# Performance work log

Hardware: AMD Instinct MI355X
Metric: run time of the kernel (lower is better)

## Reference

```python
import jax, jax.numpy as jnp
import numpy as np

INPUT_SIZE = 32   # activity vocab
HIDDEN = 512
OUT = 33          # OUT-1 activity logits + 1 duration
COND = 128
LAYERS = 2
MAXLEN = 64
BATCH = 256
SOS = 0
SLOPE = 0.01      # LeakyReLU default negative slope

def _leaky(x):
    return jnp.where(x >= 0, x, SLOPE * x)

def setup_inputs() -> dict:
    key = jax.random.key(0)
    ks = jax.random.split(key, 16)
    s = 0.05  # small init scale keeps gates in a sane range
    return {
        "batch_size": BATCH,
        "h0": jax.random.normal(ks[0], (LAYERS, BATCH, HIDDEN), jnp.float32),
        "c0": jax.random.normal(ks[1], (LAYERS, BATCH, HIDDEN), jnp.float32),
        "conditionals": jax.random.normal(ks[2], (BATCH, COND), jnp.float32),
        "emb": jax.random.normal(ks[3], (INPUT_SIZE, HIDDEN - 1), jnp.float32) * s,
        "Wih": jax.random.normal(ks[4], (LAYERS, 4 * HIDDEN, HIDDEN), jnp.float32) * s,
        "Whh": jax.random.normal(ks[5], (LAYERS, 4 * HIDDEN, HIDDEN), jnp.float32) * s,
        "bih": jax.random.normal(ks[6], (LAYERS, 4 * HIDDEN), jnp.float32) * s,
        "bhh": jax.random.normal(ks[7], (LAYERS, 4 * HIDDEN), jnp.float32) * s,
        "fcW": jax.random.normal(ks[8], (HIDDEN, COND), jnp.float32) * s,
        "fcb": jax.random.normal(ks[9], (HIDDEN,), jnp.float32) * s,
        "fc2W": jax.random.normal(ks[10], (HIDDEN, HIDDEN), jnp.float32) * s,
        "fc2b": jax.random.normal(ks[11], (HIDDEN,), jnp.float32) * s,
        "fc3W": jax.random.normal(ks[12], (OUT, HIDDEN), jnp.float32) * s,
        "fc3b": jax.random.normal(ks[13], (OUT,), jnp.float32) * s,
    }

def reference(batch_size, h0, c0, conditionals, emb, Wih, Whh, bih, bhh,
              fcW, fcb, fc2W, fc2b, fc3W, fc3b):
    B = h0.shape[1]
    # conditionals branch is step-invariant: compute once (same math as per-step fc+LeakyReLU)
    cond = _leaky(conditionals @ fcW.T + fcb)  # [B, H]
    # decoder_input = zeros[B,1,2] with act channel = sos
    inp0 = jnp.concatenate(
        [jnp.full((B, 1), float(SOS), jnp.float32), jnp.zeros((B, 1), jnp.float32)], axis=-1)

    def step(carry, _):
        h, c, inp = carry  # h,c: [L,B,H], inp: [B,2]
        # CustomDurationEmbedding: embed act index, concat duration channel -> [B,H]
        x = jnp.concatenate([emb[inp[:, 0].astype(jnp.int32)], inp[:, 1:]], axis=-1)
        hs, cs = [], []
        for l in range(LAYERS):  # seq_len==1 per step -> one LSTM cell per layer
            g = x @ Wih[l].T + bih[l] + h[l] @ Whh[l].T + bhh[l]  # [B,4H]
            i_g, f_g, g_g, o_g = jnp.split(g, 4, axis=-1)         # torch gate order i,f,g,o
            c_l = jax.nn.sigmoid(f_g) * c[l] + jax.nn.sigmoid(i_g) * jnp.tanh(g_g)
            h_l = jax.nn.sigmoid(o_g) * jnp.tanh(c_l)
            hs.append(h_l); cs.append(c_l)
            x = h_l
        h_new, c_new = jnp.stack(hs), jnp.stack(cs)
        # conditional_add: (lstm_out + cond) -> fc2 -> LeakyReLU -> fc3
        pred = _leaky((x + cond) @ fc2W.T + fc2b) @ fc3W.T + fc3b  # [B,OUT]
        # pack: topk(1) over activity logits; softmax over singleton seq dim == 1.0
        act = jnp.argmax(pred[:, :OUT - 1], axis=-1).astype(pred.dtype)[:, None]
        dur = jnp.ones((B, 1), pred.dtype)
        nxt = jnp.concatenate([act, dur], axis=-1)
        return (h_new, c_new, nxt), pred

    _, outs = jax.lax.scan(step, (h0, c0, inp0), None, length=MAXLEN)  # [T,B,OUT]
    outs = jnp.transpose(outs, (1, 0, 2))  # [B,T,OUT]
    acts_log_probs = jax.nn.log_softmax(outs[..., :OUT - 1], axis=-1)
    durations = jax.nn.softmax(outs[..., OUT - 1:], axis=1)  # Softmax(dim=-2): over time
    return jnp.concatenate([acts_log_probs, durations], axis=-1)
```

## Files before the change

### kernel.cpp

```cpp
#include <hip/hip_runtime.h>
#include <math.h>

#define BB   256
#define HH   512
#define TT   64
#define NOUT 33
#define CD   128
#define NTHR 1024
#define NWG  256
#define LOFF (4*HH*HH)
#define SZ   (HH*BB)
#define FC2OFF 4194304

typedef float f16v __attribute__((ext_vector_type(16)));
typedef const __attribute__((address_space(4))) float cfloat;
typedef const __attribute__((address_space(4))) f16v  cf16v;

__device__ __forceinline__ float sigm(float x)  { return 1.0f/(1.0f+expf(-x)); }
__device__ __forceinline__ float lrelu(float x) { return x >= 0.0f ? x : 0.01f*x; }

__device__ __forceinline__ float gld(const float* p) {
  return __hip_atomic_load(p, __ATOMIC_RELAXED, __HIP_MEMORY_SCOPE_AGENT);
}
__device__ __forceinline__ float2 gld2(const float* p) {
  unsigned long long v = __hip_atomic_load((const unsigned long long*)p,
                                           __ATOMIC_RELAXED, __HIP_MEMORY_SCOPE_AGENT);
  union { unsigned long long u; float2 f; } c; c.u = v; return c.f;
}
__device__ __forceinline__ void gst(float* p, float v) {
  __hip_atomic_store(p, v, __ATOMIC_RELAXED, __HIP_MEMORY_SCOPE_AGENT);
}
__device__ __forceinline__ unsigned gldu(const unsigned* p) {
  return __hip_atomic_load(p, __ATOMIC_RELAXED, __HIP_MEMORY_SCOPE_AGENT);
}

__device__ __forceinline__ cfloat* cptr(const float* p) {
  unsigned long long u = (unsigned long long)p;
  unsigned lo = __builtin_amdgcn_readfirstlane((unsigned)u);
  unsigned hi = __builtin_amdgcn_readfirstlane((unsigned)(u >> 32));
  return (cfloat*)((((unsigned long long)hi) << 32) | (unsigned long long)lo);
}

__device__ __forceinline__ void gbar(unsigned* bar, unsigned ep, int grp, bool fence) {
  __syncthreads();
  if (threadIdx.x == 0) {
    if (fence) __builtin_amdgcn_fence(__ATOMIC_RELEASE, "agent");
    unsigned old = __hip_atomic_fetch_add(&bar[grp*16], 1u, __ATOMIC_RELAXED, __HIP_MEMORY_SCOPE_AGENT);
    if (old == ep*32u + 31u) {
      unsigned o2 = __hip_atomic_fetch_add(&bar[128], 1u, __ATOMIC_RELAXED, __HIP_MEMORY_SCOPE_AGENT);
      if (o2 == ep*8u + 7u)
        __hip_atomic_store(&bar[144], ep+1u, __ATOMIC_RELAXED, __HIP_MEMORY_SCOPE_AGENT);
    }
    while (gldu(&bar[144]) < ep+1u) __builtin_amdgcn_s_sleep(1);
    if (fence) __builtin_amdgcn_fence(__ATOMIC_ACQUIRE, "agent");
  }
  __syncthreads();
}

extern "C" __global__ void __launch_bounds__(256)
transpose_weights(const float* __restrict__ Wih, const float* __restrict__ Whh,
                  const float* __restrict__ fc2W, float* __restrict__ wsT)
{
  const int i = blockIdx.x, tid = threadIdx.x;
  float* dst = wsT + (size_t)i*32768;
  #pragma unroll 1
  for (int idx = tid; idx < 32768; idx += 256) {
    int slot = idx & 15, k = (idx>>4)&511, rh = (idx>>13)&1, l = (idx>>14)&1;
    int a = slot>>3, r = slot&7, u = r>>2, g = r&3;
    int hu = i*4 + rh*2 + u;
    const float* src = a ? Whh : Wih;
    dst[idx] = src[(size_t)l*LOFF + (size_t)(g*HH+hu)*HH + k];
  }
  float* dstf = wsT + FC2OFF + (size_t)i*2048;
  #pragma unroll 1
  for (int idx = tid; idx < 2048; idx += 256) {
    int r = idx & 3, k = idx >> 2;
    dstf[idx] = fc2W[(size_t)(i*4+r)*HH + k];
  }
}

__device__ __forceinline__ void lstm_phase(const float* __restrict__ wTl,
    const float* __restrict__ bias, float* __restrict__ red,
    const float* __restrict__ xsrc, const float* __restrict__ hsrc,
    float* __restrict__ hdst, float& creg, int i, int j, int tid)
{
  const int lane = tid & 63, wvid = tid >> 6;
  const int rh = wvid & 1, ks = wvid >> 1;
  cf16v* wp = (cf16v*)cptr(wTl + ((size_t)rh*512 + ks*64)*16);
  const int bo = j*128 + 2*lane;
  const float* xp = xsrc + (size_t)(ks*64)*BB + bo;
  const float* hp = hsrc + (size_t)(ks*64)*BB + bo;

  float acc[16];
  #pragma unroll
  for (int r = 0; r < 16; ++r) acc[r] = 0.f;

  float2 qx[2], qh[2], px[2], ph[2], rx[2], rhb[2];
  #pragma unroll
  for (int kk = 0; kk < 2; ++kk) { qx[kk]=gld2(xp+kk*BB);     qh[kk]=gld2(hp+kk*BB); }
  #pragma unroll
  for (int kk = 0; kk < 2; ++kk) { px[kk]=gld2(xp+(2+kk)*BB); ph[kk]=gld2(hp+(2+kk)*BB); }

  #pragma unroll 1
  for (int g = 0; g < 32; ++g) {
    if (g+2 < 32) {
      #pragma unroll
      for (int kk = 0; kk < 2; ++kk) {
        rx[kk]  = gld2(xp + (g*2+4+kk)*BB);
        rhb[kk] = gld2(hp + (g*2+4+kk)*BB);
      }
    }
    #pragma unroll
    for (int kk = 0; kk < 2; ++kk) {
      f16v w = wp[g*2+kk];
      float2 xv = qx[kk], hv = qh[kk];
      #pragma unroll
      for (int r = 0; r < 8; ++r) {
        acc[r*2+0] += w[r]*xv.x + w[8+r]*hv.x;
        acc[r*2+1] += w[r]*xv.y + w[8+r]*hv.y;
      }
    }
    #pragma unroll
    for (int kk = 0; kk < 2; ++kk) {
      qx[kk]=px[kk]; qh[kk]=ph[kk]; px[kk]=rx[kk]; ph[kk]=rhb[kk];
    }
  }
  #pragma unroll
  for (int r = 0; r < 8; ++r)
    *(float2*)(red + (size_t)(ks*16 + rh*8 + r)*128 + 2*lane) = make_float2(acc[r*2], acc[r*2+1]);
  __syncthreads();
  if (tid < 512) {
    const int lhu = tid >> 7, b = tid & 127;
    float g4[4];
    #pragma unroll
    for (int gg = 0; gg < 4; ++gg) {
      float s = bias[lhu*4+gg];
      #pragma unroll
      for (int q = 0; q < 8; ++q) s += red[(q*16 + lhu*4+gg)*128 + b];
      g4[gg] = s;
    }
    float ig=sigm(g4[0]), fg=sigm(g4[1]), gv=tanhf(g4[2]), og=sigm(g4[3]);
    float cn = fg*creg + ig*gv;
    creg = cn;
    gst(hdst + (size_t)(i*4+lhu)*BB + j*128 + b, og*tanhf(cn));
  }
}

__device__ __forceinline__ void fc2_phase(const float* __restrict__ h2src,
    const float* __restrict__ wsTf, float* __restrict__ yb,
    const float* lds_bc, const float* condY_l, float* __restrict__ red,
    int i, int j, int tid)
{
  const int lane = tid & 63, ks2 = tid >> 6;
  cf16v* wp = (cf16v*)cptr(wsTf + (size_t)ks2*128);
  const int bo = j*128 + 2*lane;
  const float* hp = h2src + (size_t)(ks2*32)*BB + bo;
  float acc[8];
  #pragma unroll
  for (int r = 0; r < 8; ++r) acc[r] = 0.f;
  float2 qh[4], ph[4];
  #pragma unroll
  for (int kk = 0; kk < 4; ++kk) qh[kk] = gld2(hp + kk*BB);
  #pragma unroll 1
  for (int g = 0; g < 8; ++g) {
    if (g+1 < 8) {
      #pragma unroll
      for (int kk = 0; kk < 4; ++kk) ph[kk] = gld2(hp + (g*4+4+kk)*BB);
    }
    f16v w = wp[g];
    #pragma unroll
    for (int kk = 0; kk < 4; ++kk) {
      float2 hv = qh[kk];
      #pragma unroll
      for (int r = 0; r < 4; ++r) {
        acc[r*2+0] += w[kk*4+r]*hv.x;
        acc[r*2+1] += w[kk*4+r]*hv.y;
      }
    }
    #pragma unroll
    for (int kk = 0; kk < 4; ++kk) qh[kk] = ph[kk];
  }
  #pragma unroll
  for (int r = 0; r < 4; ++r)
    *(float2*)(red + (size_t)(ks2*4+r)*128 + 2*lane) = make_float2(acc[r*2], acc[r*2+1]);
  __syncthreads();
  if (tid < 512) {
    int r = tid >> 7, b = tid & 127;
    float s = lds_bc[r] + condY_l[r*128+b];
    #pragma unroll
    for (int q = 0; q < 16; ++q) s += red[(q*4+r)*128 + b];
    gst(yb + (size_t)(i*4+r)*BB + j*128 + b, lrelu(s));
  }
}

extern "C" __global__ void __launch_bounds__(NTHR)
decoder_kernel(const float* __restrict__ h0, const float* __restrict__ c0,
               const float* __restrict__ conds, const float* __restrict__ emb,
               const float* __restrict__ wsTW, const float* __restrict__ bih,
               const float* __restrict__ bhh, const float* __restrict__ fcW,
               const float* __restrict__ fcb, const float* __restrict__ fc2W,
               const float* __restrict__ fc2b, const float* __restrict__ fc3W,
               const float* __restrict__ fc3b,
               float* __restrict__ out, unsigned* bar, float* wsf)
{
  const int w = blockIdx.x;
  const int i = w & 127, j = w >> 7;
  const int grp = w & 7;
  const int tid = threadIdx.x;

  float* xbuf  = wsf;
  float* h1a = wsf + 1*SZ;  float* h1b = wsf + 2*SZ;
  float* h2a = wsf + 3*SZ;  float* h2b = wsf + 4*SZ;
  float* yb  = wsf + 5*SZ;
  float* condb = wsf + 6*SZ;
  const float* wTi  = wsTW + (size_t)i*32768;
  const float* wsTf = wsTW + FC2OFF + (size_t)i*2048;

  __shared__ float red[16384];
  __shared__ float lds_y[HH];
  __shared__ float part[NOUT][17];
  __shared__ float condY_l[512];
  __shared__ float lds_b1[16], lds_b2[16], lds_bc[4];
  __shared__ int   lds_act;
  __shared__ float lds_pad[3072];
  if (tid == 0) ((volatile float*)lds_pad)[0] = 0.f;

  if (tid < 16) {
    int u2 = tid >> 2, g = tid & 3;
    int hu = i*4 + u2;
    lds_b1[tid] = bih[g*HH+hu] + bhh[g*HH+hu];
    lds_b2[tid] = bih[4*HH + g*HH+hu] + bhh[4*HH + g*HH+hu];
  }
  if (tid < 4) lds_bc[tid] = fc2b[i*4 + tid];

  {
    int u = tid >> 8, b = tid & 255;
    int hug = i*4 + u;
    h1a[(size_t)hug*BB + b] = h0[(size_t)b*HH + hug];
    h2a[(size_t)hug*BB + b] = h0[(size_t)(BB+b)*HH + hug];
    xbuf[(size_t)hug*BB + b] = (hug < HH-1) ? emb[hug] : 0.0f;
    const float* crow = conds + (size_t)b*CD;
    cfloat* fr = cptr(fcW + (size_t)hug*CD);
    float s = fcb[hug];
    #pragma unroll 4
    for (int q = 0; q < CD; q += 4)
      s += fr[q]*crow[q] + fr[q+1]*crow[q+1] + fr[q+2]*crow[q+2] + fr[q+3]*crow[q+3];
    condb[(size_t)hug*BB + b] = lrelu(s);
  }
  float c1 = 0.f, c2 = 0.f;
  if (tid < 512) {
    int lhu = tid >> 7, b = tid & 127;
    int hug = i*4 + lhu, bg = j*128 + b;
    c1 = c0[(size_t)bg*HH + hug];
    c2 = c0[(size_t)(BB+bg)*HH + hug];
  }
  unsigned ep = 0;
  gbar(bar, ep++, grp, true);

  if (tid < 512) {
    int r = tid >> 7, b = tid & 127, bg = j*128 + b;
    cfloat* wr = cptr(fc2W + (size_t)(i*4+r)*HH);
    float s = 0.f;
    #pragma unroll 4
    for (int k = 0; k < HH; ++k) s += wr[k]*condb[(size_t)k*BB + bg];
    condY_l[r*128 + b] = s;
  }
  __syncthreads();

  for (int t = 0; t < TT; ++t) {
    float* h1r = (t&1) ? h1b : h1a;  float* h1w = (t&1) ? h1a : h1b;
    float* h2r = (t&1) ? h2b : h2a;  float* h2w = (t&1) ? h2a : h2b;

    lstm_phase(wTi,         lds_b1, red, xbuf, h1r, h1w, c1, i, j, tid);
    gbar(bar, ep++, grp, false);
    lstm_phase(wTi + 16384, lds_b2, red, h1w, h2r, h2w, c2, i, j, tid);
    gbar(bar, ep++, grp, false);
    fc2_phase(h2w, wsTf, yb, lds_bc, condY_l, red, i, j, tid);
    gbar(bar, ep++, grp, false);
    {
      if (tid < 512) lds_y[tid] = gld(yb + (size_t)tid*BB + w);
      __syncthreads();
      int o = 0, kc = 0;
      bool active = false;
      if (tid < 512)      { o = tid & 31; kc = tid >> 5; active = true; }
      else if (tid < 528) { o = 32;       kc = tid - 512; active = true; }
      if (active) {
        float p = 0.f;
        const float* fw = fc3W + (size_t)o*HH + kc*32;
        #pragma unroll
        for (int k2 = 0; k2 < 32; ++k2) p += fw[k2] * lds_y[kc*32 + k2];
        part[o][kc] = p;
      }
      __syncthreads();
      float predv = -1e30f;
      if (tid < NOUT) {
        float s = fc3b[tid];
        #pragma unroll
        for (int kc2 = 0; kc2 < 16; ++kc2) s += part[tid][kc2];
        predv = s;
        out[(size_t)(w*TT + t)*NOUT + tid] = s;
      }
      if (tid < 64) {
        float v  = (tid < 32) ? predv : -1e30f;
        int  idx = tid;
        #pragma unroll
        for (int off = 32; off > 0; off >>= 1) {
          float ov = __shfl_xor(v, off);
          int   oi = __shfl_xor(idx, off);
          if (ov > v || (ov == v && oi < idx)) { v = ov; idx = oi; }
        }
        if (tid == 0) lds_act = idx;
      }
      __syncthreads();
      const int act = lds_act;
      if (tid < 512)
        gst(xbuf + (size_t)tid*BB + w, (tid < HH-1) ? emb[(size_t)act*(HH-1) + tid] : 1.0f);
    }
    gbar(bar, ep++, grp, false);
  }

  if (tid < TT) {
    const int s = tid;
    float* po = out + (size_t)(w*TT + s)*NOUT;
    float v[NOUT];
    #pragma unroll
    for (int o = 0; o < NOUT; ++o) v[o] = po[o];
    float m = v[0];
    #pragma unroll
    for (int o = 1; o < 32; ++o) m = fmaxf(m, v[o]);
    float sum = 0.f;
    #pragma unroll
    for (int o = 0; o < 32; ++o) sum += expf(v[o] - m);
    float lse = m + logf(sum);
    #pragma unroll
    for (int o = 0; o < 32; ++o) po[o] = v[o] - lse;
    float d = v[32];
    float dm = d;
    #pragma unroll
    for (int off = 32; off > 0; off >>= 1) dm = fmaxf(dm, __shfl_xor(dm, off));
    float e = expf(d - dm);
    float es = e;
    #pragma unroll
    for (int off = 32; off > 0; off >>= 1) es += __shfl_xor(es, off);
    po[32] = e / es;
  }
}

extern "C" void kernel_launch(void* const* d_in, const int* in_sizes, int n_in,
                              void* d_out, int out_size, void* d_ws, size_t ws_size,
                              hipStream_t stream) {
  const float* h0   = (const float*)d_in[1];
  const float* c0   = (const float*)d_in[2];
  const float* cnd  = (const float*)d_in[3];
  const float* emb  = (const float*)d_in[4];
  const float* Wih  = (const float*)d_in[5];
  const float* Whh  = (const float*)d_in[6];
  const float* bih  = (const float*)d_in[7];
  const float* bhh  = (const float*)d_in[8];
  const float* fcW  = (const float*)d_in[9];
  const float* fcb  = (const float*)d_in[10];
  const float* fc2W = (const float*)d_in[11];
  const float* fc2b = (const float*)d_in[12];
  const float* fc3W = (const float*)d_in[13];
  const float* fc3b = (const float*)d_in[14];

  unsigned* bar = (unsigned*)d_ws;
  float* wsf = (float*)((char*)d_ws + 1024);
  float* wsT = wsf + 7*SZ;

  (void)hipMemsetAsync(d_ws, 0, 1024, stream);

  hipLaunchKernelGGL(transpose_weights, dim3(128), dim3(256), 0, stream,
                     Wih, Whh, fc2W, wsT);
  hipLaunchKernelGGL(decoder_kernel, dim3(NWG), dim3(NTHR), 0, stream,
                     h0, c0, cnd, emb, wsT, bih, bhh, fcW, fcb,
                     fc2W, fc2b, fc3W, fc3b, (float*)d_out, bar, wsf);
}
```

Measured before the change: 4.567 ms.

## Give each wave all 16 gate rows over a 32-wide K slice in LSTM matvec

The LSTM phase stops splitting gate rows across two waves. Each of 16 waves now computes all 16 gate rows for a 32-element K slice, which halves the redundant x/h activation loads per wave. The weight transpose layout is changed to match, and the reduction now sums 16 partials instead of 8, so the LDS red buffer doubles to 128KB. The fc2 phase is reworked to stream 8-float weight vectors with a two-row h prefetch. The cost is 32 accumulators per thread, more register pressure, and a larger LDS footprint in place of the old padding array.

```diff
diff --git a/kernel.cpp b/kernel.cpp
--- a/kernel.cpp
+++ b/kernel.cpp
@@ -13,8 +13,10 @@
 #define FC2OFF 4194304
 
 typedef float f16v __attribute__((ext_vector_type(16)));
+typedef float f8v  __attribute__((ext_vector_type(8)));
 typedef const __attribute__((address_space(4))) float cfloat;
 typedef const __attribute__((address_space(4))) f16v  cf16v;
+typedef const __attribute__((address_space(4))) f8v   cf8v;
 
 __device__ __forceinline__ float sigm(float x)  { return 1.0f/(1.0f+expf(-x)); }
 __device__ __forceinline__ float lrelu(float x) { return x >= 0.0f ? x : 0.01f*x; }
@@ -65,9 +67,9 @@
   float* dst = wsT + (size_t)i*32768;
   #pragma unroll 1
   for (int idx = tid; idx < 32768; idx += 256) {
-    int slot = idx & 15, k = (idx>>4)&511, rh = (idx>>13)&1, l = (idx>>14)&1;
-    int a = slot>>3, r = slot&7, u = r>>2, g = r&3;
-    int hu = i*4 + rh*2 + u;
+    int slot = idx & 31, k = (idx>>5)&511, l = idx>>14;
+    int a = slot>>4, r = slot&15, u = r>>2, g = r&3;
+    int hu = i*4 + u;
     const float* src = a ? Whh : Wih;
     dst[idx] = src[(size_t)l*LOFF + (size_t)(g*HH+hu)*HH + k];
   }
@@ -84,50 +86,47 @@
     const float* __restrict__ xsrc, const float* __restrict__ hsrc,
     float* __restrict__ hdst, float& creg, int i, int j, int tid)
 {
-  const int lane = tid & 63, wvid = tid >> 6;
-  const int rh = wvid & 1, ks = wvid >> 1;
-  cf16v* wp = (cf16v*)cptr(wTl + ((size_t)rh*512 + ks*64)*16);
+  const int lane = tid & 63, ks = tid >> 6;
+  cf16v* wp = (cf16v*)cptr(wTl + (size_t)(ks*32)*32);
   const int bo = j*128 + 2*lane;
-  const float* xp = xsrc + (size_t)(ks*64)*BB + bo;
-  const float* hp = hsrc + (size_t)(ks*64)*BB + bo;
-
-  float acc[16];
+  const float* xp = xsrc + (size_t)(ks*32)*BB + bo;
+  const float* hp = hsrc + (size_t)(ks*32)*BB + bo;
+
+  float acc[32];
   #pragma unroll
-  for (int r = 0; r < 16; ++r) acc[r] = 0.f;
-
-  float2 qx[2], qh[2], px[2], ph[2], rx[2], rhb[2];
+  for (int r = 0; r < 32; ++r) acc[r] = 0.f;
+
+  float2 qx0, qh0, qx1, qh1, nx0, nh0, nx1, nh1;
+  qx0 = gld2(xp);      qh0 = gld2(hp);
+  qx1 = gld2(xp + BB); qh1 = gld2(hp + BB);
+
+  #pragma unroll 1
+  for (int it = 0; it < 16; ++it) {
+    if (it+1 < 16) {
+      nx0 = gld2(xp + (2*it+2)*BB); nh0 = gld2(hp + (2*it+2)*BB);
+      nx1 = gld2(xp + (2*it+3)*BB); nh1 = gld2(hp + (2*it+3)*BB);
+    }
+    {
+      f16v wi = wp[it*4+0], wh = wp[it*4+1];
+      #pragma unroll
+      for (int r = 0; r < 16; ++r) {
+        acc[2*r]   += wi[r]*qx0.x + wh[r]*qh0.x;
+        acc[2*r+1] += wi[r]*qx0.y + wh[r]*qh0.y;
+      }
+    }
+    {
+      f16v wi = wp[it*4+2], wh = wp[it*4+3];
+      #pragma unroll
+      for (int r = 0; r < 16; ++r) {
+        acc[2*r]   += wi[r]*qx1.x + wh[r]*qh1.x;
+        acc[2*r+1] += wi[r]*qx1.y + wh[r]*qh1.y;
+      }
+    }
+    qx0 = nx0; qh0 = nh0; qx1 = nx1; qh1 = nh1;
+  }
   #pragma unroll
-  for (int kk = 0; kk < 2; ++kk) { qx[kk]=gld2(xp+kk*BB);     qh[kk]=gld2(hp+kk*BB); }
-  #pragma unroll
-  for (int kk = 0; kk < 2; ++kk) { px[kk]=gld2(xp+(2+kk)*BB); ph[kk]=gld2(hp+(2+kk)*BB); }
-
-  #pragma unroll 1
-  for (int g = 0; g < 32; ++g) {
-    if (g+2 < 32) {
-      #pragma unroll
-      for (int kk = 0; kk < 2; ++kk) {
-        rx[kk]  = gld2(xp + (g*2+4+kk)*BB);
-        rhb[kk] = gld2(hp + (g*2+4+kk)*BB);
-      }
-    }
-    #pragma unroll
-    for (int kk = 0; kk < 2; ++kk) {
-      f16v w = wp[g*2+kk];
-      float2 xv = qx[kk], hv = qh[kk];
-      #pragma unroll
-      for (int r = 0; r < 8; ++r) {
-        acc[r*2+0] += w[r]*xv.x + w[8+r]*hv.x;
-        acc[r*2+1] += w[r]*xv.y + w[8+r]*hv.y;
-      }
-    }
-    #pragma unroll
-    for (int kk = 0; kk < 2; ++kk) {
-      qx[kk]=px[kk]; qh[kk]=ph[kk]; px[kk]=rx[kk]; ph[kk]=rhb[kk];
-    }
-  }
-  #pragma unroll
-  for (int r = 0; r < 8; ++r)
-    *(float2*)(red + (size_t)(ks*16 + rh*8 + r)*128 + 2*lane) = make_float2(acc[r*2], acc[r*2+1]);
+  for (int r = 0; r < 16; ++r)
+    *(float2*)(red + (size_t)(ks*16 + r)*128 + 2*lane) = make_float2(acc[2*r], acc[2*r+1]);
   __syncthreads();
   if (tid < 512) {
     const int lhu = tid >> 7, b = tid & 127;
@@ -136,7 +135,7 @@
     for (int gg = 0; gg < 4; ++gg) {
       float s = bias[lhu*4+gg];
       #pragma unroll
-      for (int q = 0; q < 8; ++q) s += red[(q*16 + lhu*4+gg)*128 + b];
+      for (int q = 0; q < 16; ++q) s += red[(size_t)(q*16 + lhu*4+gg)*128 + b];
       g4[gg] = s;
     }
     float ig=sigm(g4[0]), fg=sigm(g4[1]), gv=tanhf(g4[2]), og=sigm(g4[3]);
@@ -151,44 +150,38 @@
     const float* lds_bc, const float* condY_l, float* __restrict__ red,
     int i, int j, int tid)
 {
-  const int lane = tid & 63, ks2 = tid >> 6;
-  cf16v* wp = (cf16v*)cptr(wsTf + (size_t)ks2*128);
+  const int lane = tid & 63, ks = tid >> 6;
+  cf8v* wpf = (cf8v*)cptr(wsTf + (size_t)ks*128);
   const int bo = j*128 + 2*lane;
-  const float* hp = h2src + (size_t)(ks2*32)*BB + bo;
+  const float* hp = h2src + (size_t)(ks*32)*BB + bo;
   float acc[8];
   #pragma unroll
   for (int r = 0; r < 8; ++r) acc[r] = 0.f;
-  float2 qh[4], ph[4];
-  #pragma unroll
-  for (int kk = 0; kk < 4; ++kk) qh[kk] = gld2(hp + kk*BB);
+  float2 qh0, qh1, nh0, nh1;
+  qh0 = gld2(hp); qh1 = gld2(hp + BB);
   #pragma unroll 1
-  for (int g = 0; g < 8; ++g) {
-    if (g+1 < 8) {
-      #pragma unroll
-      for (int kk = 0; kk < 4; ++kk) ph[kk] = gld2(hp + (g*4+4+kk)*BB);
-    }
-    f16v w = wp[g];
-    #pragma unroll
-    for (int kk = 0; kk < 4; ++kk) {
-      float2 hv = qh[kk];
-      #pragma unroll
-      for (int r = 0; r < 4; ++r) {
-        acc[r*2+0] += w[kk*4+r]*hv.x;
-        acc[r*2+1] += w[kk*4+r]*hv.y;
-      }
-    }
-    #pragma unroll
-    for (int kk = 0; kk < 4; ++kk) qh[kk] = ph[kk];
+  for (int it = 0; it < 16; ++it) {
+    if (it+1 < 16) {
+      nh0 = gld2(hp + (2*it+2)*BB);
+      nh1 = gld2(hp + (2*it+3)*BB);
+    }
+    f8v w = wpf[it];
+    #pragma unroll
+    for (int r = 0; r < 4; ++r) {
+      acc[2*r]   += w[r]*qh0.x + w[4+r]*qh1.x;
+      acc[2*r+1] += w[r]*qh0.y + w[4+r]*qh1.y;
+    }
+    qh0 = nh0; qh1 = nh1;
   }
   #pragma unroll
   for (int r = 0; r < 4; ++r)
-    *(float2*)(red + (size_t)(ks2*4+r)*128 + 2*lane) = make_float2(acc[r*2], acc[r*2+1]);
+    *(float2*)(red + (size_t)(ks*4+r)*128 + 2*lane) = make_float2(acc[2*r], acc[2*r+1]);
   __syncthreads();
   if (tid < 512) {
     int r = tid >> 7, b = tid & 127;
     float s = lds_bc[r] + condY_l[r*128+b];
     #pragma unroll
-    for (int q = 0; q < 16; ++q) s += red[(q*4+r)*128 + b];
+    for (int q = 0; q < 16; ++q) s += red[(size_t)(q*4+r)*128 + b];
     gst(yb + (size_t)(i*4+r)*BB + j*128 + b, lrelu(s));
   }
 }
@@ -216,14 +209,12 @@
   const float* wTi  = wsTW + (size_t)i*32768;
   const float* wsTf = wsTW + FC2OFF + (size_t)i*2048;
 
-  __shared__ float red[16384];
+  __shared__ float red[32768];
   __shared__ float lds_y[HH];
   __shared__ float part[NOUT][17];
   __shared__ float condY_l[512];
   __shared__ float lds_b1[16], lds_b2[16], lds_bc[4];
   __shared__ int   lds_act;
-  __shared__ float lds_pad[3072];
-  if (tid == 0) ((volatile float*)lds_pad)[0] = 0.f;
 
   if (tid < 16) {
     int u2 = tid >> 2, g = tid & 3;
```

After: 4.062 ms. 11.1% less time.
